# Performance work log

Measured on AMD Instinct MI355X. Metric: run time of the kernel, lower is better.

Reference implementation:

```python
import jax, jax.numpy as jnp
import numpy as np

N_NODES = 50000
N_EDGES = 800000
F_IN = 512
NHID = 256
N_CLASSES = 10
N_GRAPHS = 64


def setup_inputs() -> dict:
    key = jax.random.key(0)
    ks = jax.random.split(key, 8)
    x = jax.random.normal(ks[0], (N_NODES, F_IN), dtype=jnp.float32)
    edge_index = jax.random.randint(ks[1], (2, N_EDGES), 0, N_NODES, dtype=jnp.int32)
    # sorted graph-assignment covering all N_GRAPHS segments (global max pool ids)
    batch = ((jnp.arange(N_NODES) * N_GRAPHS) // N_NODES).astype(jnp.int32)
    s1 = 1.0 / np.sqrt(F_IN)
    s2 = 1.0 / np.sqrt(NHID)
    W1 = jax.random.normal(ks[2], (F_IN, NHID), dtype=jnp.float32) * s1
    W2 = jax.random.normal(ks[3], (NHID, NHID), dtype=jnp.float32) * s2
    W3 = jax.random.normal(ks[4], (NHID, NHID), dtype=jnp.float32) * s2
    Wl = jax.random.normal(ks[5], (NHID, N_CLASSES), dtype=jnp.float32) * s2
    b1 = jnp.zeros((NHID,), jnp.float32)
    b2 = jnp.zeros((NHID,), jnp.float32)
    b3 = jnp.zeros((NHID,), jnp.float32)
    bl = jnp.zeros((N_CLASSES,), jnp.float32)
    return dict(x=x, edge_index=edge_index, batch=batch,
                W1=W1, b1=b1, W2=W2, b2=b2, W3=W3, b3=b3, Wl=Wl, bl=bl)


def reference(x, edge_index, batch, W1, b1, W2, b2, W3, b3, Wl, bl):
    n = x.shape[0]
    loop = jnp.arange(n, dtype=edge_index.dtype)
    src = jnp.concatenate([edge_index[0], loop])  # [E+N]
    dst = jnp.concatenate([edge_index[1], loop])
    # symmetric GCN normalization with self-loops: deg >= 1
    deg = jax.ops.segment_sum(jnp.ones_like(dst, jnp.float32), dst, num_segments=n)
    dinv = jax.lax.rsqrt(deg)
    norm = dinv[src] * dinv[dst]  # [E+N]

    def gcn(h, W, b):
        hw = h @ W                                   # [N, H] dense GEMM
        msg = hw[src] * norm[:, None]                # gather + scale [E+N, H]
        agg = jax.ops.segment_sum(msg, dst, num_segments=n)  # scatter-add
        return agg + b

    h = jax.nn.relu(gcn(x, W1, b1))
    h = jax.nn.relu(gcn(h, W2, b2))
    h = jax.nn.relu(gcn(h, W3, b3))
    g = jax.ops.segment_max(h, batch, num_segments=N_GRAPHS)  # global max pool [G, H]
    return jax.nn.log_softmax(g @ Wl + bl, axis=-1)
```

## Files before the change

kernel.cpp:

```cpp
#include <hip/hip_runtime.h>
#include <hip/hip_bf16.h>
#include <cstdint>
#include <cstddef>

typedef __attribute__((ext_vector_type(8))) short short8;
typedef __attribute__((ext_vector_type(4))) float f32x4;

__device__ __forceinline__ unsigned short f32_to_bf16_rn(float f) {
  unsigned int u = __float_as_uint(f);
  u += 0x7FFFu + ((u >> 16) & 1u);
  return (unsigned short)(u >> 16);
}
__device__ __forceinline__ float bf16_to_f32(unsigned short b) {
  return __uint_as_float(((unsigned int)b) << 16);
}
__device__ __forceinline__ void split_bf(float f, unsigned short& hi, unsigned short& lo) {
  hi = f32_to_bf16_rn(f);
  lo = f32_to_bf16_rn(f - bf16_to_f32(hi));
}
__device__ __forceinline__ float4 bf4_to_f4(ushort4 v) {
  float4 r;
  r.x = bf16_to_f32(v.x); r.y = bf16_to_f32(v.y);
  r.z = bf16_to_f32(v.z); r.w = bf16_to_f32(v.w);
  return r;
}

__global__ void k_init(int* cnt, int* cursor, float* g, int M, int GH) {
  int i = blockIdx.x * blockDim.x + threadIdx.x;
  int stride = gridDim.x * blockDim.x;
  for (int x = i; x < M; x += stride) { cnt[x] = 0; cursor[x] = 0; }
  for (int x = i; x < GH; x += stride) g[x] = 0.f;
}

__global__ void k_count(const int* __restrict__ dst, int* __restrict__ cnt, int E) {
  int i = blockIdx.x * blockDim.x + threadIdx.x;
  for (int e = i; e < E; e += gridDim.x * blockDim.x)
    atomicAdd(&cnt[dst[e]], 1);
}

__global__ void k_dinv(const int* __restrict__ cnt, float* __restrict__ dinv, int M) {
  int i = blockIdx.x * blockDim.x + threadIdx.x;
  if (i < M) dinv[i] = rsqrtf((float)(cnt[i] + 1));
}

__global__ void k_scan1(const int* __restrict__ cnt, int* __restrict__ excl,
                        int* __restrict__ bsum, int M) {
  __shared__ int s[256];
  int gid = blockIdx.x * 256 + threadIdx.x;
  int v = (gid < M) ? cnt[gid] : 0;
  s[threadIdx.x] = v;
  __syncthreads();
  for (int off = 1; off < 256; off <<= 1) {
    int t = (threadIdx.x >= off) ? s[threadIdx.x - off] : 0;
    __syncthreads();
    s[threadIdx.x] += t;
    __syncthreads();
  }
  if (gid < M) excl[gid] = s[threadIdx.x] - v;
  if (threadIdx.x == 255) bsum[blockIdx.x] = s[255];
}

__global__ void k_scan2(int* bsum, int nb) {
  __shared__ int s[256];
  int v = (threadIdx.x < nb) ? bsum[threadIdx.x] : 0;
  s[threadIdx.x] = v;
  __syncthreads();
  for (int off = 1; off < 256; off <<= 1) {
    int t = (threadIdx.x >= off) ? s[threadIdx.x - off] : 0;
    __syncthreads();
    s[threadIdx.x] += t;
    __syncthreads();
  }
  if (threadIdx.x < nb) bsum[threadIdx.x] = s[threadIdx.x] - v;
}

__global__ void k_scan3(int* row_ptr, const int* __restrict__ bsum, int M, int E) {
  int gid = blockIdx.x * 256 + threadIdx.x;
  if (gid < M) row_ptr[gid] += bsum[blockIdx.x];
  if (gid == 0) row_ptr[M] = E;
}

__global__ void k_scatter(const int* __restrict__ src, const int* __restrict__ dst,
                          const int* __restrict__ row_ptr, int* __restrict__ cursor,
                          int* __restrict__ eidx, int E) {
  int i = blockIdx.x * blockDim.x + threadIdx.x;
  for (int e = i; e < E; e += gridDim.x * blockDim.x) {
    int d = dst[e];
    int pos = atomicAdd(&cursor[d], 1);
    eidx[row_ptr[d] + pos] = src[e];
  }
}

__global__ void k_wtrans(const float* __restrict__ W, unsigned short* __restrict__ WTh,
                         unsigned short* __restrict__ WTl, int K) {
  int idx = blockIdx.x * 256 + threadIdx.x;
  if (idx >= K * 256) return;
  int n = idx / K, k = idx % K;
  float v = W[(size_t)k * 256 + n];
  unsigned short h, l;
  split_bf(v, h, l);
  WTh[(size_t)n * K + k] = h;
  WTl[(size_t)n * K + k] = l;
}

#define BM 64
#define BN 256
#define BK 32

__device__ __forceinline__ int swz(int row, int k) {
  return row * BK + (((((k >> 3) ^ (row >> 1)) & 3) << 3) | (k & 7));
}

template <bool AF32>
__global__ __launch_bounds__(256) void k_gemm(
    const float* __restrict__ Af,
    const unsigned short* __restrict__ Ahg, const unsigned short* __restrict__ Alg,
    const unsigned short* __restrict__ WTh, const unsigned short* __restrict__ WTl,
    const float* __restrict__ dinv, unsigned short* __restrict__ out, int M, int K) {
  __shared__ __align__(16) unsigned short Ah[BM * BK], Al[BM * BK];
  __shared__ __align__(16) unsigned short Bh[BN * BK], Bl[BN * BK];
  const int tid = threadIdx.x;
  const int lane = tid & 63;
  const int wv = tid >> 6;
  const int row0 = blockIdx.x * BM;

  f32x4 acc[4][4] = {};

  const int arow = tid >> 2;
  const int achk = tid & 3;

  for (int k0 = 0; k0 < K; k0 += BK) {
    {
      int gr = row0 + arow;
      int off = swz(arow, achk * 8);
      if constexpr (AF32) {
        float f[8];
        if (gr < M) {
          const float* p = Af + (size_t)gr * K + k0 + achk * 8;
          float4 v0 = *(const float4*)p;
          float4 v1 = *(const float4*)(p + 4);
          f[0] = v0.x; f[1] = v0.y; f[2] = v0.z; f[3] = v0.w;
          f[4] = v1.x; f[5] = v1.y; f[6] = v1.z; f[7] = v1.w;
        } else {
#pragma unroll
          for (int i = 0; i < 8; i++) f[i] = 0.f;
        }
        short8 hv, lv;
#pragma unroll
        for (int i = 0; i < 8; i++) {
          unsigned short h, l;
          split_bf(f[i], h, l);
          hv[i] = (short)h; lv[i] = (short)l;
        }
        *(short8*)&Ah[off] = hv;
        *(short8*)&Al[off] = lv;
      } else {
        short8 vh, vl;
        if (gr < M) {
          vh = *(const short8*)(Ahg + (size_t)gr * K + k0 + achk * 8);
          vl = *(const short8*)(Alg + (size_t)gr * K + k0 + achk * 8);
        } else {
          vh = (short8)(short)0; vl = (short8)(short)0;
        }
        *(short8*)&Ah[off] = vh;
        *(short8*)&Al[off] = vl;
      }
    }
#pragma unroll
    for (int it = 0; it < 4; ++it) {
      int idx = tid + it * 256;
      int col = idx >> 2, chk = idx & 3;
      short8 vh = *(const short8*)(WTh + (size_t)col * K + k0 + chk * 8);
      short8 vl = *(const short8*)(WTl + (size_t)col * K + k0 + chk * 8);
      int off = swz(col, chk * 8);
      *(short8*)&Bh[off] = vh;
      *(short8*)&Bl[off] = vl;
    }
    __syncthreads();
    const int fr = lane & 15;
    const int kq = (lane >> 4) * 8;
    short8 ah[4], al[4];
#pragma unroll
    for (int m = 0; m < 4; ++m) {
      int off = swz(m * 16 + fr, kq);
      ah[m] = *(const short8*)&Ah[off];
      al[m] = *(const short8*)&Al[off];
    }
#pragma unroll
    for (int n = 0; n < 4; ++n) {
      int off = swz(wv * 64 + n * 16 + fr, kq);
      short8 bh = *(const short8*)&Bh[off];
      short8 bl = *(const short8*)&Bl[off];
#pragma unroll
      for (int m = 0; m < 4; ++m) {
        acc[m][n] = __builtin_amdgcn_mfma_f32_16x16x32_bf16(ah[m], bh, acc[m][n], 0, 0, 0);
        acc[m][n] = __builtin_amdgcn_mfma_f32_16x16x32_bf16(ah[m], bl, acc[m][n], 0, 0, 0);
        acc[m][n] = __builtin_amdgcn_mfma_f32_16x16x32_bf16(al[m], bh, acc[m][n], 0, 0, 0);
      }
    }
    __syncthreads();
  }
  const int fr = lane & 15;
  const int rq = (lane >> 4) * 4;
#pragma unroll
  for (int m = 0; m < 4; ++m) {
#pragma unroll
    for (int r = 0; r < 4; ++r) {
      int gr = row0 + m * 16 + rq + r;
      if (gr < M) {
        float s = dinv[gr];
#pragma unroll
        for (int n = 0; n < 4; ++n)
          out[(size_t)gr * BN + wv * 64 + n * 16 + fr] = f32_to_bf16_rn(acc[m][n][r] * s);
      }
    }
  }
}

__global__ __launch_bounds__(64) void k_aggregate(
    const unsigned short* __restrict__ hws, const int* __restrict__ eidx,
    const int* __restrict__ row_ptr, const float* __restrict__ dinv,
    const float* __restrict__ bias, unsigned short* __restrict__ out_hi,
    unsigned short* __restrict__ out_lo, float* __restrict__ out_f32, int M) {
  int i = blockIdx.x;
  if (i >= M) return;
  int t = threadIdx.x;
  float4 acc = bf4_to_f4(*(const ushort4*)(hws + (size_t)i * 256 + t * 4));
  int beg = row_ptr[i], end = row_ptr[i + 1];
  int e = beg;
  for (; e + 4 <= end; e += 4) {
    int s0 = eidx[e + 0], s1 = eidx[e + 1], s2 = eidx[e + 2], s3 = eidx[e + 3];
    ushort4 v0 = *(const ushort4*)(hws + (size_t)s0 * 256 + t * 4);
    ushort4 v1 = *(const ushort4*)(hws + (size_t)s1 * 256 + t * 4);
    ushort4 v2 = *(const ushort4*)(hws + (size_t)s2 * 256 + t * 4);
    ushort4 v3 = *(const ushort4*)(hws + (size_t)s3 * 256 + t * 4);
    float4 f0 = bf4_to_f4(v0), f1 = bf4_to_f4(v1);
    float4 f2 = bf4_to_f4(v2), f3 = bf4_to_f4(v3);
    acc.x += (f0.x + f1.x) + (f2.x + f3.x);
    acc.y += (f0.y + f1.y) + (f2.y + f3.y);
    acc.z += (f0.z + f1.z) + (f2.z + f3.z);
    acc.w += (f0.w + f1.w) + (f2.w + f3.w);
  }
  for (; e < end; ++e) {
    int s = eidx[e];
    float4 v = bf4_to_f4(*(const ushort4*)(hws + (size_t)s * 256 + t * 4));
    acc.x += v.x; acc.y += v.y; acc.z += v.z; acc.w += v.w;
  }
  float d = dinv[i];
  float4 b = *(const float4*)(bias + t * 4);
  float r[4];
  r[0] = fmaxf(fmaf(acc.x, d, b.x), 0.f);
  r[1] = fmaxf(fmaf(acc.y, d, b.y), 0.f);
  r[2] = fmaxf(fmaf(acc.z, d, b.z), 0.f);
  r[3] = fmaxf(fmaf(acc.w, d, b.w), 0.f);
  if (out_f32) {
    float4 o; o.x = r[0]; o.y = r[1]; o.z = r[2]; o.w = r[3];
    *(float4*)(out_f32 + (size_t)i * 256 + t * 4) = o;
  } else {
    ushort4 hv, lv;
    unsigned short h, l;
    split_bf(r[0], h, l); hv.x = h; lv.x = l;
    split_bf(r[1], h, l); hv.y = h; lv.y = l;
    split_bf(r[2], h, l); hv.z = h; lv.z = l;
    split_bf(r[3], h, l); hv.w = h; lv.w = l;
    *(ushort4*)(out_hi + (size_t)i * 256 + t * 4) = hv;
    *(ushort4*)(out_lo + (size_t)i * 256 + t * 4) = lv;
  }
}

__global__ __launch_bounds__(256) void k_pool(const float* __restrict__ h,
                                              const int* __restrict__ batch,
                                              float* __restrict__ g, int M) {
  int node0 = blockIdx.x * 32;
  if (node0 >= M) return;
  int t = threadIdx.x;
  int nEnd = min(node0 + 32, M);
  int cur = batch[node0];
  float acc = 0.f;
  for (int n = node0; n < nEnd; ++n) {
    int b = batch[n];
    if (b != cur) {
      atomicMax((int*)&g[(size_t)cur * 256 + t], __float_as_int(acc));
      acc = 0.f; cur = b;
    }
    acc = fmaxf(acc, h[(size_t)n * 256 + t]);
  }
  atomicMax((int*)&g[(size_t)cur * 256 + t], __float_as_int(acc));
}

__global__ __launch_bounds__(256) void k_classify(const float* __restrict__ g,
                                                  const float* __restrict__ Wl,
                                                  const float* __restrict__ bl,
                                                  float* __restrict__ out) {
  __shared__ float sg[256];
  __shared__ float logits[10];
  int b = blockIdx.x;
  sg[threadIdx.x] = g[(size_t)b * 256 + threadIdx.x];
  __syncthreads();
  if (threadIdx.x < 10) {
    float s = bl[threadIdx.x];
    for (int k = 0; k < 256; ++k) s = fmaf(sg[k], Wl[k * 10 + threadIdx.x], s);
    logits[threadIdx.x] = s;
  }
  __syncthreads();
  if (threadIdx.x == 0) {
    float m = logits[0];
    for (int c = 1; c < 10; c++) m = fmaxf(m, logits[c]);
    float sum = 0.f;
    for (int c = 0; c < 10; c++) sum += expf(logits[c] - m);
    float lse = m + logf(sum);
    for (int c = 0; c < 10; c++) out[b * 10 + c] = logits[c] - lse;
  }
}

static inline size_t align256(size_t x) { return (x + 255) & ~(size_t)255; }

extern "C" void kernel_launch(void* const* d_in, const int* in_sizes, int n_in,
                              void* d_out, int out_size, void* d_ws, size_t ws_size,
                              hipStream_t stream) {
  const float* x   = (const float*)d_in[0];
  const int*   ei  = (const int*)d_in[1];
  const int*   bat = (const int*)d_in[2];
  const float* W1  = (const float*)d_in[3];
  const float* b1  = (const float*)d_in[4];
  const float* W2  = (const float*)d_in[5];
  const float* b2  = (const float*)d_in[6];
  const float* W3  = (const float*)d_in[7];
  const float* b3  = (const float*)d_in[8];
  const float* Wl  = (const float*)d_in[9];
  const float* bl  = (const float*)d_in[10];
  float* out = (float*)d_out;

  const int M = in_sizes[0] / 512;
  const int E = in_sizes[1] / 2;
  const int G = out_size / 10;
  const int K1 = 512, H = 256;

  const int* src = ei;
  const int* dst = ei + E;

  char* p = (char*)d_ws;
  size_t off = 0;
  float* p_dinv = (float*)(p + off); off = align256(off + (size_t)M * 4);
  int* cnt      = (int*)(p + off);   off = align256(off + (size_t)M * 4);
  int* cursor   = (int*)(p + off);   off = align256(off + (size_t)M * 4);
  int* row_ptr  = (int*)(p + off);   off = align256(off + ((size_t)M + 1) * 4);
  int* bsum     = (int*)(p + off);   off = align256(off + 256 * 4);
  int* eidx     = (int*)(p + off);   off = align256(off + (size_t)E * 4);
  float* g      = (float*)(p + off); off = align256(off + (size_t)G * H * 4);
  unsigned short* WT1h = (unsigned short*)(p + off); off = align256(off + (size_t)H * K1 * 2);
  unsigned short* WT1l = (unsigned short*)(p + off); off = align256(off + (size_t)H * K1 * 2);
  unsigned short* WT2h = (unsigned short*)(p + off); off = align256(off + (size_t)H * H * 2);
  unsigned short* WT2l = (unsigned short*)(p + off); off = align256(off + (size_t)H * H * 2);
  unsigned short* WT3h = (unsigned short*)(p + off); off = align256(off + (size_t)H * H * 2);
  unsigned short* WT3l = (unsigned short*)(p + off); off = align256(off + (size_t)H * H * 2);
  unsigned short* hws = (unsigned short*)(p + off); off = align256(off + (size_t)M * H * 2);
  unsigned short* h_hi = (unsigned short*)(p + off); off += (size_t)M * H * 2;
  unsigned short* h_lo = (unsigned short*)(p + off); off = align256(off + (size_t)M * H * 2);
  float* bufC = (float*)h_hi;
  (void)ws_size;

  int nb = (M + 255) / 256;

  k_init<<<256, 256, 0, stream>>>(cnt, cursor, g, M, G * H);
  k_count<<<1024, 256, 0, stream>>>(dst, cnt, E);
  k_dinv<<<nb, 256, 0, stream>>>(cnt, p_dinv, M);
  k_scan1<<<nb, 256, 0, stream>>>(cnt, row_ptr, bsum, M);
  k_scan2<<<1, 256, 0, stream>>>(bsum, nb);
  k_scan3<<<nb, 256, 0, stream>>>(row_ptr, bsum, M, E);
  k_scatter<<<1024, 256, 0, stream>>>(src, dst, row_ptr, cursor, eidx, E);

  k_wtrans<<<(H * K1 + 255) / 256, 256, 0, stream>>>(W1, WT1h, WT1l, K1);
  k_wtrans<<<(H * H + 255) / 256, 256, 0, stream>>>(W2, WT2h, WT2l, H);
  k_wtrans<<<(H * H + 255) / 256, 256, 0, stream>>>(W3, WT3h, WT3l, H);

  int gblk = (M + BM - 1) / BM;
  k_gemm<true><<<gblk, 256, 0, stream>>>(x, nullptr, nullptr, WT1h, WT1l, p_dinv, hws, M, K1);
  k_aggregate<<<M, 64, 0, stream>>>(hws, eidx, row_ptr, p_dinv, b1, h_hi, h_lo, nullptr, M);
  k_gemm<false><<<gblk, 256, 0, stream>>>(nullptr, h_hi, h_lo, WT2h, WT2l, p_dinv, hws, M, H);
  k_aggregate<<<M, 64, 0, stream>>>(hws, eidx, row_ptr, p_dinv, b2, h_hi, h_lo, nullptr, M);
  k_gemm<false><<<gblk, 256, 0, stream>>>(nullptr, h_hi, h_lo, WT3h, WT3l, p_dinv, hws, M, H);
  k_aggregate<<<M, 64, 0, stream>>>(hws, eidx, row_ptr, p_dinv, b3, nullptr, nullptr, bufC, M);

  k_pool<<<(M + 31) / 32, 256, 0, stream>>>(bufC, bat, g, M);
  k_classify<<<G, 256, 0, stream>>>(g, Wl, bl, out);
}
```

Baseline: 587.6 us.

## Load GEMM tiles directly into LDS with global_load_lds

Replaces the register-staged global-to-LDS copies in the GEMM with direct global_load_lds 16-byte transfers, using precomputed per-lane source pointers and swizzled LDS slots. For the fp32 input layer, the raw fp32 tile is staged in LDS and then split into bf16 hi/lo planes, which adds an extra barrier. The goal is to cut VGPR pressure and load/store instruction overhead in the GEMM. Out-of-range rows are now clamped to M-1 instead of being zero-filled, and the load is still synchronous with no double buffering.

Result: no change. 598.5 us (+1.9%).

```diff
diff --git a/kernel.cpp b/kernel.cpp
--- a/kernel.cpp
+++ b/kernel.cpp
@@ -23,6 +23,12 @@
   r.x = bf16_to_f32(v.x); r.y = bf16_to_f32(v.y);
   r.z = bf16_to_f32(v.z); r.w = bf16_to_f32(v.w);
   return r;
+}
+
+__device__ __forceinline__ void gload16(const void* g, const void* l) {
+  __builtin_amdgcn_global_load_lds(
+      (const __attribute__((address_space(1))) unsigned int*)g,
+      (__attribute__((address_space(3))) unsigned int*)l, 16, 0, 0);
 }
 
 __global__ void k_init(int* cnt, int* cursor, float* g, int M, int GH) {
@@ -107,90 +113,100 @@
 #define BN 256
 #define BK 32
 
-__device__ __forceinline__ int swz(int row, int k) {
-  return row * BK + (((((k >> 3) ^ (row >> 1)) & 3) << 3) | (k & 7));
-}
-
 template <bool AF32>
 __global__ __launch_bounds__(256) void k_gemm(
     const float* __restrict__ Af,
     const unsigned short* __restrict__ Ahg, const unsigned short* __restrict__ Alg,
     const unsigned short* __restrict__ WTh, const unsigned short* __restrict__ WTl,
     const float* __restrict__ dinv, unsigned short* __restrict__ out, int M, int K) {
-  __shared__ __align__(16) unsigned short Ah[BM * BK], Al[BM * BK];
-  __shared__ __align__(16) unsigned short Bh[BN * BK], Bl[BN * BK];
+  constexpr int AHB = AF32 ? 8192 : 0;
+  constexpr int ALB = AHB + 4096;
+  constexpr int BHB = AF32 ? 16384 : 8192;
+  constexpr int BLB = BHB + 16384;
+  constexpr int LDSZ = BLB + 16384;
+  __shared__ __align__(16) char lds[LDSZ];
+
   const int tid = threadIdx.x;
   const int lane = tid & 63;
   const int wv = tid >> 6;
   const int row0 = blockIdx.x * BM;
+  const int ASTEP = AF32 ? BK * 4 : BK * 2;
+
+  const char* gsrc[10];
+  unsigned ldsoff[10];
+#pragma unroll
+  for (int i = 0; i < 10; ++i) {
+    int c = wv + 4 * i;
+    if (i < 2) {
+      ldsoff[i] = (unsigned)(c * 1024);
+      if constexpr (AF32) {
+        int r = c * 8 + (lane >> 3);
+        int sslot = (lane & 7) ^ (r & 7);
+        int gr = row0 + r; gr = gr < M ? gr : (M - 1);
+        gsrc[i] = (const char*)(Af + (size_t)gr * K + sslot * 4);
+      } else {
+        int plane = c >> 2;
+        int r = (c & 3) * 16 + (lane >> 2);
+        int sslot = (lane & 3) ^ ((r >> 1) & 3);
+        int gr = row0 + r; gr = gr < M ? gr : (M - 1);
+        const unsigned short* base = plane ? Alg : Ahg;
+        gsrc[i] = (const char*)(base + (size_t)gr * K + sslot * 8);
+      }
+    } else {
+      int cb = c - 8;
+      ldsoff[i] = (unsigned)(BHB + cb * 1024);
+      int plane = cb >> 4;
+      int col = (cb & 15) * 16 + (lane >> 2);
+      int sslot = (lane & 3) ^ ((col >> 1) & 3);
+      const unsigned short* base = plane ? WTl : WTh;
+      gsrc[i] = (const char*)(base + (size_t)col * K + sslot * 8);
+    }
+  }
 
   f32x4 acc[4][4] = {};
-
-  const int arow = tid >> 2;
-  const int achk = tid & 3;
+  const int fr = lane & 15;
+  const int ks = lane >> 4;
 
   for (int k0 = 0; k0 < K; k0 += BK) {
-    {
-      int gr = row0 + arow;
-      int off = swz(arow, achk * 8);
-      if constexpr (AF32) {
-        float f[8];
-        if (gr < M) {
-          const float* p = Af + (size_t)gr * K + k0 + achk * 8;
-          float4 v0 = *(const float4*)p;
-          float4 v1 = *(const float4*)(p + 4);
-          f[0] = v0.x; f[1] = v0.y; f[2] = v0.z; f[3] = v0.w;
-          f[4] = v1.x; f[5] = v1.y; f[6] = v1.z; f[7] = v1.w;
-        } else {
-#pragma unroll
-          for (int i = 0; i < 8; i++) f[i] = 0.f;
-        }
-        short8 hv, lv;
-#pragma unroll
-        for (int i = 0; i < 8; i++) {
-          unsigned short h, l;
-          split_bf(f[i], h, l);
-          hv[i] = (short)h; lv[i] = (short)l;
-        }
-        *(short8*)&Ah[off] = hv;
-        *(short8*)&Al[off] = lv;
-      } else {
-        short8 vh, vl;
-        if (gr < M) {
-          vh = *(const short8*)(Ahg + (size_t)gr * K + k0 + achk * 8);
-          vl = *(const short8*)(Alg + (size_t)gr * K + k0 + achk * 8);
-        } else {
-          vh = (short8)(short)0; vl = (short8)(short)0;
-        }
-        *(short8*)&Ah[off] = vh;
-        *(short8*)&Al[off] = vl;
+#pragma unroll
+    for (int i = 0; i < 10; ++i) {
+      gload16(gsrc[i], lds + ldsoff[i]);
+      gsrc[i] += (i < 2) ? ASTEP : (BK * 2);
+    }
+    __syncthreads();
+
+    if constexpr (AF32) {
+      int r = tid >> 2, q = tid & 3, rx = r & 7;
+      float4 f0 = *(const float4*)&lds[(size_t)r * 128 + (((2 * q) ^ rx) * 16)];
+      float4 f1 = *(const float4*)&lds[(size_t)r * 128 + (((2 * q + 1) ^ rx) * 16)];
+      float f[8] = {f0.x, f0.y, f0.z, f0.w, f1.x, f1.y, f1.z, f1.w};
+      short8 hv, lv;
+#pragma unroll
+      for (int j = 0; j < 8; ++j) {
+        unsigned short h, l;
+        split_bf(f[j], h, l);
+        hv[j] = (short)h; lv[j] = (short)l;
       }
-    }
-#pragma unroll
-    for (int it = 0; it < 4; ++it) {
-      int idx = tid + it * 256;
-      int col = idx >> 2, chk = idx & 3;
-      short8 vh = *(const short8*)(WTh + (size_t)col * K + k0 + chk * 8);
-      short8 vl = *(const short8*)(WTl + (size_t)col * K + k0 + chk * 8);
-      int off = swz(col, chk * 8);
-      *(short8*)&Bh[off] = vh;
-      *(short8*)&Bl[off] = vl;
-    }
-    __syncthreads();
-    const int fr = lane & 15;
-    const int kq = (lane >> 4) * 8;
+      int so = (q ^ ((r >> 1) & 3)) * 16;
+      *(short8*)&lds[AHB + r * 64 + so] = hv;
+      *(short8*)&lds[ALB + r * 64 + so] = lv;
+      __syncthreads();
+    }
+
     short8 ah[4], al[4];
 #pragma unroll
     for (int m = 0; m < 4; ++m) {
-      int off = swz(m * 16 + fr, kq);
-      ah[m] = *(const short8*)&Ah[off];
-      al[m] = *(const short8*)&Al[off];
+      int rr = m * 16 + fr;
+      int so = (ks ^ ((rr >> 1) & 3)) * 16;
+      ah[m] = *(const short8*)&lds[AHB + rr * 64 + so];
+      al[m] = *(const short8*)&lds[ALB + rr * 64 + so];
     }
 #pragma unroll
     for (int n = 0; n < 4; ++n) {
-      int off = swz(wv * 64 + n * 16 + fr, kq);
-      short8 bh = *(const short8*)&Bh[off];
-      short8 bl = *(const short8*)&Bl[off];
+      int cc = wv * 64 + n * 16 + fr;
+      int so = (ks ^ ((cc >> 1) & 3)) * 16;
+      short8 bh = *(const short8*)&lds[BHB + cc * 64 + so];
+      short8 bl = *(const short8*)&lds[BLB + cc * 64 + so];
 #pragma unroll
       for (int m = 0; m < 4; ++m) {
         acc[m][n] = __builtin_amdgcn_mfma_f32_16x16x32_bf16(ah[m], bh, acc[m][n], 0, 0, 0);
@@ -200,7 +216,7 @@
     }
     __syncthreads();
   }
-  const int fr = lane & 15;
+
   const int rq = (lane >> 4) * 4;
 #pragma unroll
   for (int m = 0; m < 4; ++m) {
```
